# Kernel tuning notes

Hardware: AMD Instinct MI355X
Metric: run time of the kernel (lower is better)

The kernel has to match this reference:

```python
import jax, jax.numpy as jnp
import numpy as np

B, T, C = 2, 2048, 1024
H = 16
D = C // H  # head_dim = 64


def setup_inputs() -> dict:
    key = jax.random.key(0)
    k1, k2, k3, k4, k5 = jax.random.split(key, 5)
    s = 1.0 / np.sqrt(C)
    return {
        "x": jax.random.normal(k1, (B, T, C), dtype=jnp.float32),
        "w_qkv": jax.random.normal(k2, (C, 3 * C), dtype=jnp.float32) * s,
        "b_qkv": jax.random.normal(k3, (3 * C,), dtype=jnp.float32) * 0.01,
        "w_out": jax.random.normal(k4, (C, C), dtype=jnp.float32) * s,
        "b_out": jax.random.normal(k5, (C,), dtype=jnp.float32) * 0.01,
    }


def reference(x, w_qkv, b_qkv, w_out, b_out):
    Bx, Tx, Cx = x.shape
    qkv = x @ w_qkv + b_qkv                      # [B,T,3C]
    qkv = qkv.reshape(Bx, Tx, 3, H, D)
    q, k, v = qkv[:, :, 0], qkv[:, :, 1], qkv[:, :, 2]  # [B,T,H,D]
    # [B,H,T,T] scores with scaling
    scores = jnp.einsum("bqhd,bkhd->bhqk", q, k) / np.sqrt(D).astype(np.float32)
    causal = jnp.tril(jnp.ones((Tx, Tx), dtype=bool))
    scores = jnp.where(causal[None, None], scores, -jnp.inf)
    attn = jax.nn.softmax(scores, axis=-1)
    out = jnp.einsum("bhqk,bkhd->bqhd", attn, v).reshape(Bx, Tx, Cx)
    return out @ w_out + b_out
```

## Files before the change

kernel.cpp:

```cpp
#include <hip/hip_runtime.h>
#include <stdint.h>

typedef unsigned short u16;
typedef __attribute__((ext_vector_type(8))) short bfrag;
typedef __attribute__((ext_vector_type(4))) short bfrag4;
typedef __attribute__((ext_vector_type(4))) float f32x4;

#define MFMA_BF16 __builtin_amdgcn_mfma_f32_16x16x32_bf16

static constexpr int Bc = 2;
static constexpr int Tc = 2048;
static constexpr int Cc = 1024;
static constexpr int Hc = 16;
static constexpr int Dc = 64;
static constexpr int N3 = 3 * Cc;

__device__ __forceinline__ u16 f2bf(float f) {
    union { unsigned int i; float f; } v; v.f = f;
    unsigned int u = v.i;
    u += 0x7fffu + ((u >> 16) & 1u);
    return (u16)(u >> 16);
}
__device__ __forceinline__ unsigned int fbits(float f) {
    union { unsigned int i; float f; } v; v.f = f; return v.i;
}
__device__ __forceinline__ unsigned int pack_bf2(float hi, float lo) {
    return __builtin_amdgcn_perm(fbits(hi), fbits(lo), 0x07060302u);
}

#if __has_builtin(__builtin_amdgcn_mfma_f32_16x16x16bf16_1k)
__device__ __forceinline__ f32x4 MFMA16(bfrag4 a, bfrag4 b, f32x4 c) {
    return __builtin_amdgcn_mfma_f32_16x16x16bf16_1k(a, b, c, 0, 0, 0);
}
#elif __has_builtin(__builtin_amdgcn_mfma_f32_16x16x16_bf16)
__device__ __forceinline__ f32x4 MFMA16(bfrag4 a, bfrag4 b, f32x4 c) {
    return __builtin_amdgcn_mfma_f32_16x16x16_bf16(a, b, c, 0, 0, 0);
}
#else
__device__ __forceinline__ f32x4 MFMA16(bfrag4 a, bfrag4 b, f32x4 c) {
    bfrag a8 = {a[0], a[1], a[2], a[3], 0, 0, 0, 0};
    bfrag b8 = {b[0], b[1], b[2], b[3], 0, 0, 0, 0};
    return MFMA_BF16(a8, b8, c, 0, 0, 0);
}
#endif

__device__ __forceinline__ void async_load16(const u16* g, u16* lds) {
    __builtin_amdgcn_global_load_lds(
        (const __attribute__((address_space(1))) unsigned int*)g,
        (__attribute__((address_space(3))) unsigned int*)lds, 16, 0, 0);
}

__global__ __launch_bounds__(256) void prep(
    const float* __restrict__ x, const float* __restrict__ w_qkv,
    const float* __restrict__ w_out, u16* __restrict__ xb,
    u16* __restrict__ WqkvT, u16* __restrict__ WoutT) {
    __shared__ u16 tile[32][33];
    const int blk = blockIdx.x, tid = threadIdx.x;
    if (blk < 4096) {
        const int i = (blk * 256 + tid) * 4;
        const float4 v = *(const float4*)(x + i);
        ushort4 o;
        o.x = f2bf(v.x); o.y = f2bf(v.y); o.z = f2bf(v.z); o.w = f2bf(v.w);
        *(ushort4*)(xb + i) = o;
        return;
    }
    const float* in; u16* out; int rows, cols, c0, r0;
    if (blk < 4096 + 3072) {
        const int t = blk - 4096;
        in = w_qkv; out = WqkvT; rows = 1024; cols = 3072;
        c0 = (t % 96) * 32; r0 = (t / 96) * 32;
    } else {
        const int t = blk - 7168;
        in = w_out; out = WoutT; rows = 1024; cols = 1024;
        c0 = (t & 31) * 32; r0 = (t >> 5) * 32;
    }
    const int row = tid >> 3;
    const int cg  = (tid & 7) * 4;
    const float4 v = *(const float4*)(in + (size_t)(r0 + row) * cols + c0 + cg);
    tile[cg + 0][row] = f2bf(v.x);
    tile[cg + 1][row] = f2bf(v.y);
    tile[cg + 2][row] = f2bf(v.z);
    tile[cg + 3][row] = f2bf(v.w);
    __syncthreads();
    const int tx = tid & 31, ty = tid >> 5;
    for (int i = 0; i < 4; i++)
        out[(size_t)(c0 + ty + 8 * i) * rows + r0 + tx] = tile[ty + 8 * i][tx];
}

__global__ __launch_bounds__(512, 2) void gemm_qkv(
    const u16* __restrict__ A, const u16* __restrict__ BT,
    const float* __restrict__ bias, u16* __restrict__ outQK,
    u16* __restrict__ Vt) {
    constexpr int Kd = 1024, Nn = 3072, Td = 32;
    extern __shared__ __align__(16) u16 smem[];
    u16* As = smem;
    u16* Bs = smem + 4 * (128 * 32);

    const int tid  = threadIdx.x;
    const int wave = tid >> 6, lane = tid & 63;
    const int quad = lane >> 4, l16 = lane & 15;
    const int wm = wave >> 2, wn = wave & 3;
    const int m0 = blockIdx.y * 128, n0 = blockIdx.x * 384;

    f32x4 acc[4][6];
    #pragma unroll
    for (int i = 0; i < 4; i++)
        #pragma unroll
        for (int j = 0; j < 6; j++)
            acc[i][j] = (f32x4){0.f, 0.f, 0.f, 0.f};

    const int rloc = 2 * (lane >> 3) + ((lane >> 2) & 1);
    const int cg   = ((lane & 3) ^ ((lane >> 3) & 3)) * 8;
    const int rk   = (l16 >> 1) & 3;
    const int rodd = (l16 & 1) * 32;

    const u16* Ag = A  + (size_t)(m0 + wave * 16 + rloc) * Kd + cg;
    const u16* Bg = BT + (size_t)(n0 + wave * 48 + rloc) * Kd + cg;
    u16* ldsA = As + (wave * 16) * 32;
    u16* ldsB = Bs + (wave * 48) * 32;

    int offA[4], offB[6];
    #pragma unroll
    for (int mt = 0; mt < 4; mt++) {
        const int r = wm * 64 + mt * 16 + l16;
        offA[mt] = (r >> 1) * 64 + rodd + (quad ^ rk) * 8;
    }
    #pragma unroll
    for (int nt = 0; nt < 6; nt++) {
        const int r = wn * 96 + nt * 16 + l16;
        offB[nt] = (r >> 1) * 64 + rodd + (quad ^ rk) * 8;
    }

    #define GLD_A(h, bsel)                                                     \
        async_load16(Ag + ((h) << 5), ldsA + (bsel) * (128 * 32));
    #define GLD_B(h, bsel, j)                                                  \
        async_load16(Bg + (size_t)((j) * 16) * Kd + ((h) << 5),                \
                     ldsB + (bsel) * (384 * 32) + (j) * (16 * 32));

    #pragma unroll
    for (int h = 0; h < 3; h++) {
        GLD_A(h, h);
        GLD_B(h, h, 0); GLD_B(h, h, 1); GLD_B(h, h, 2);
    }
    asm volatile("s_waitcnt vmcnt(8)" ::: "memory");
    __builtin_amdgcn_s_barrier();
    asm volatile("" ::: "memory");

    for (int h = 0; h < Td; h++) {
        const int bsel = h & 3;
        const u16* Ab = As + bsel * (128 * 32);
        const u16* Bb = Bs + bsel * (384 * 32);
        const int psel = (h + 3) & 3;

        bfrag af[4], bf0[3];
        #pragma unroll
        for (int mt = 0; mt < 4; mt++) af[mt] = *(const bfrag*)(Ab + offA[mt]);
        #pragma unroll
        for (int nt = 0; nt < 3; nt++) bf0[nt] = *(const bfrag*)(Bb + offB[nt]);
        if (h + 3 < Td) { GLD_A(h + 3, psel); GLD_B(h + 3, psel, 0); }
        __builtin_amdgcn_s_barrier();
        asm volatile("s_waitcnt lgkmcnt(0)" ::: "memory");
        __builtin_amdgcn_sched_barrier(0);
        __builtin_amdgcn_s_setprio(1);
        #pragma unroll
        for (int mt = 0; mt < 4; mt++)
            #pragma unroll
            for (int nt = 0; nt < 3; nt++)
                acc[mt][nt] = MFMA_BF16(af[mt], bf0[nt], acc[mt][nt], 0, 0, 0);
        __builtin_amdgcn_s_setprio(0);
        __builtin_amdgcn_s_barrier();
        asm volatile("" ::: "memory");

        bfrag bf1[3];
        #pragma unroll
        for (int nt = 0; nt < 3; nt++)
            bf1[nt] = *(const bfrag*)(Bb + offB[nt + 3]);
        if (h + 3 < Td) { GLD_B(h + 3, psel, 1); GLD_B(h + 3, psel, 2); }
        if (h <= Td - 4)      asm volatile("s_waitcnt vmcnt(8)" ::: "memory");
        else if (h == Td - 3) asm volatile("s_waitcnt vmcnt(4)" ::: "memory");
        else if (h == Td - 2) asm volatile("s_waitcnt vmcnt(0)" ::: "memory");
        __builtin_amdgcn_s_barrier();
        asm volatile("s_waitcnt lgkmcnt(0)" ::: "memory");
        __builtin_amdgcn_sched_barrier(0);
        __builtin_amdgcn_s_setprio(1);
        #pragma unroll
        for (int mt = 0; mt < 4; mt++)
            #pragma unroll
            for (int nt = 0; nt < 3; nt++)
                acc[mt][nt + 3] = MFMA_BF16(af[mt], bf1[nt], acc[mt][nt + 3], 0, 0, 0);
        __builtin_amdgcn_s_setprio(0);
        __builtin_amdgcn_s_barrier();
        asm volatile("" ::: "memory");
    }
    #undef GLD_A
    #undef GLD_B

    #pragma unroll
    for (int nt = 0; nt < 6; nt++) {
        const int gn = n0 + wn * 96 + nt * 16 + l16;
        const float bv = bias[gn];
        if (gn < 2 * Cc) {
            const float scl = (gn < Cc) ? 0.125f : 1.0f;
            #pragma unroll
            for (int mt = 0; mt < 4; mt++) {
                #pragma unroll
                for (int r = 0; r < 4; r++) {
                    const int gm = m0 + wm * 64 + mt * 16 + quad * 4 + r;
                    outQK[(size_t)gm * Nn + gn] = f2bf((acc[mt][nt][r] + bv) * scl);
                }
            }
        } else {
            const int gnv = gn - 2 * Cc;
            const int h = gnv >> 6, d = gnv & 63;
            #pragma unroll
            for (int mt = 0; mt < 4; mt++) {
                const int gmb = m0 + wm * 64 + mt * 16 + quad * 4;
                const int b = gmb >> 11, trow = gmb & (Tc - 1);
                ushort4 o;
                o.x = f2bf(acc[mt][nt][0] + bv);
                o.y = f2bf(acc[mt][nt][1] + bv);
                o.z = f2bf(acc[mt][nt][2] + bv);
                o.w = f2bf(acc[mt][nt][3] + bv);
                *(ushort4*)(Vt + ((size_t)((b * Hc + h) * Dc + d)) * Tc + trow) = o;
            }
        }
    }
}

__global__ __launch_bounds__(512, 2) void gemm_out(
    const u16* __restrict__ A, const u16* __restrict__ BT,
    const float* __restrict__ bias, float* __restrict__ out,
    int M, int Nn, int K) {
    extern __shared__ __align__(16) u16 smem[];
    u16* As = smem;
    u16* Bs = smem + 3 * (128 * 32);

    const int tid  = threadIdx.x;
    const int wave = tid >> 6, lane = tid & 63;
    const int quad = lane >> 4, l16 = lane & 15;
    const int wm = wave >> 2, wn = wave & 3;
    const int m0 = blockIdx.y * 128, n0 = blockIdx.x * 128;

    f32x4 acc[4][2];
    #pragma unroll
    for (int i = 0; i < 4; i++)
        #pragma unroll
        for (int j = 0; j < 2; j++)
            acc[i][j] = (f32x4){0.f, 0.f, 0.f, 0.f};

    const int rA = lane >> 2;
    const int cA = ((lane & 3) ^ (rA & 3)) * 8;

    const u16* Ag = A  + (size_t)(m0 + wave * 16 + rA) * K + cA;
    const u16* Bg = BT + (size_t)(n0 + wave * 16 + rA) * K + cA;
    u16* ldsA = As + (wave * 16) * 32;
    u16* ldsB = Bs + (wave * 16) * 32;

    const int swz8 = (quad ^ (l16 & 3)) * 8;
    int offA[4], offB[2];
    #pragma unroll
    for (int mt = 0; mt < 4; mt++)
        offA[mt] = (wm * 64 + mt * 16 + l16) * 32 + swz8;
    #pragma unroll
    for (int nt = 0; nt < 2; nt++)
        offB[nt] = (wn * 32 + nt * 16 + l16) * 32 + swz8;

    #define STAGE_O(t, bsel)                                                   \
        {                                                                      \
            const int k0_ = (t) << 5;                                          \
            async_load16(Ag + k0_, ldsA + (bsel) * (128 * 32));                \
            async_load16(Bg + k0_, ldsB + (bsel) * (128 * 32));                \
        }

    STAGE_O(0, 0);
    STAGE_O(1, 1);

    const int T = K >> 5;
    for (int t = 0; t < T; t++) {
        if (t + 1 < T) asm volatile("s_waitcnt vmcnt(2)" ::: "memory");
        else           asm volatile("s_waitcnt vmcnt(0)" ::: "memory");
        __builtin_amdgcn_s_barrier();
        asm volatile("" ::: "memory");
        if (t + 2 < T) { STAGE_O(t + 2, (t + 2) % 3); }

        const u16* Ab = As + (t % 3) * (128 * 32);
        const u16* Bb = Bs + (t % 3) * (128 * 32);
        bfrag af[4], bf[2];
        #pragma unroll
        for (int mt = 0; mt < 4; mt++) af[mt] = *(const bfrag*)(Ab + offA[mt]);
        #pragma unroll
        for (int nt = 0; nt < 2; nt++) bf[nt] = *(const bfrag*)(Bb + offB[nt]);

        __builtin_amdgcn_s_setprio(1);
        #pragma unroll
        for (int mt = 0; mt < 4; mt++)
            #pragma unroll
            for (int nt = 0; nt < 2; nt++)
                acc[mt][nt] = MFMA_BF16(af[mt], bf[nt], acc[mt][nt], 0, 0, 0);
        __builtin_amdgcn_s_setprio(0);
    }
    #undef STAGE_O

    #pragma unroll
    for (int nt = 0; nt < 2; nt++) {
        const int gn = n0 + wn * 32 + nt * 16 + l16;
        const float bv = bias[gn];
        #pragma unroll
        for (int mt = 0; mt < 4; mt++) {
            #pragma unroll
            for (int r = 0; r < 4; r++) {
                const int gm = m0 + wm * 64 + mt * 16 + quad * 4 + r;
                out[(size_t)gm * Nn + gn] = acc[mt][nt][r] + bv;
            }
        }
    }
}

__global__ __launch_bounds__(256, 4) void attn_kernel(
    const u16* __restrict__ QKVp, const u16* __restrict__ Vt,
    u16* __restrict__ Ob) {
    __shared__ __align__(16) u16 KsF[2][64 * 64];
    __shared__ __align__(16) u16 VsF[2][64 * 64];

    const int tid  = threadIdx.x;
    const int wave = tid >> 6, lane = tid & 63;
    const int quad = lane >> 4, l16 = lane & 15;

    const int bh = blockIdx.x & 31;
    const int g5 = blockIdx.x >> 5;
    const int jq = (g5 < 8) ? 31 - g5
                 : (g5 < 16) ? g5 + 8
                 : (g5 < 24) ? 31 - g5
                 : g5 - 24;
    const int b = bh >> 4, h = bh & 15;
    const u16* Qp = QKVp + (size_t)b * Tc * N3 + h * Dc;
    const u16* Kp = Qp + Cc;
    const u16* Vp = Vt + (size_t)bh * Dc * Tc;

    const int qw = jq * 64 + wave * 16;

    const int row8 = lane >> 3;
    const int swz  = ((lane & 7) ^ row8) * 8;
    const int pk0 = ((quad)     ^ (l16 & 7)) * 8;
    const int pk1 = ((quad + 4) ^ (l16 & 7)) * 8;

    bfrag qf0, qf1;
    {
        const u16* qp = Qp + (size_t)(qw + l16) * N3 + quad * 8;
        qf0 = *(const bfrag*)qp;
        qf1 = *(const bfrag*)(qp + 32);
    }

    float l_i = 0.f;
    f32x4 oacc[4];
    #pragma unroll
    for (int g = 0; g < 4; g++) oacc[g] = (f32x4){0.f, 0.f, 0.f, 0.f};

    #define STAGEKV(t, bsel)                                                    \
        {                                                                       \
            const int k0_ = (t) * 64;                                           \
            _Pragma("unroll")                                                   \
            for (int j = 0; j < 2; j++) {                                       \
                const int rr = wave * 16 + j * 8;                               \
                const int gr = rr + row8;                                       \
                async_load16(Kp + (size_t)(k0_ + gr) * N3 + swz,                \
                             &KsF[bsel][rr * 64]);                              \
                async_load16(Vp + (size_t)gr * Tc + k0_ + swz,                  \
                             &VsF[bsel][rr * 64]);                              \
            }                                                                   \
        }

    STAGEKV(0, 0);
    for (int t = 0; t <= jq; t++) {
        __syncthreads();
        if (t < jq) STAGEKV(t + 1, (t + 1) & 1);
        const u16* Kb = KsF[t & 1];
        const u16* Vb = VsF[t & 1];

        f32x4 s[4];
        __builtin_amdgcn_s_setprio(1);
        #pragma unroll
        for (int g = 0; g < 4; g++) {
            const u16* kb = Kb + (g * 16 + l16) * 64;
            bfrag kf0 = *(const bfrag*)(kb + pk0);
            bfrag kf1 = *(const bfrag*)(kb + pk1);
            f32x4 z = (f32x4){0.f, 0.f, 0.f, 0.f};
            z = MFMA_BF16(kf0, qf0, z, 0, 0, 0);
            z = MFMA_BF16(kf1, qf1, z, 0, 0, 0);
            s[g] = z;
        }
        __builtin_amdgcn_s_setprio(0);

        #pragma unroll
        for (int g = 0; g < 4; g++)
            #pragma unroll
            for (int r = 0; r < 4; r++)
                s[g][r] = __expf(s[g][r]);
        if (t == jq) {
            #pragma unroll
            for (int g = 0; g < 4; g++)
                #pragma unroll
                for (int r = 0; r < 4; r++)
                    if (g * 16 + quad * 4 + r > wave * 16 + l16) s[g][r] = 0.f;
        }
        #pragma unroll
        for (int g = 0; g < 4; g++)
            l_i += s[g][0] + s[g][1] + s[g][2] + s[g][3];

        __builtin_amdgcn_s_setprio(1);
        #pragma unroll
        for (int g = 0; g < 4; g++) {
            union { unsigned int u[2]; bfrag4 v; } pf;
            pf.u[0] = pack_bf2(s[g][1], s[g][0]);
            pf.u[1] = pack_bf2(s[g][3], s[g][2]);
            const int vc = ((2 * g + (quad >> 1)) ^ (l16 & 7)) * 8 + (quad & 1) * 4;
            #pragma unroll
            for (int ng = 0; ng < 4; ng++) {
                const bfrag4 vf = *(const bfrag4*)(Vb + (ng * 16 + l16) * 64 + vc);
                oacc[ng] = MFMA16(vf, pf.v, oacc[ng]);
            }
        }
        __builtin_amdgcn_s_setprio(0);
    }
    #undef STAGEKV

    float rs = l_i;
    rs += __shfl_xor(rs, 16);
    rs += __shfl_xor(rs, 32);
    const float inv = 1.f / rs;
    const int q = qw + l16;
    u16* orow = Ob + (size_t)(b * Tc + q) * Cc + h * Dc + quad * 4;
    #pragma unroll
    for (int ng = 0; ng < 4; ng++) {
        ushort4 o;
        o.x = f2bf(oacc[ng][0] * inv);
        o.y = f2bf(oacc[ng][1] * inv);
        o.z = f2bf(oacc[ng][2] * inv);
        o.w = f2bf(oacc[ng][3] * inv);
        *(ushort4*)(orow + ng * 16) = o;
    }
}

extern "C" void kernel_launch(void* const* d_in, const int* in_sizes, int n_in,
                              void* d_out, int out_size, void* d_ws, size_t ws_size,
                              hipStream_t stream) {
    const float* x     = (const float*)d_in[0];
    const float* w_qkv = (const float*)d_in[1];
    const float* b_qkv = (const float*)d_in[2];
    const float* w_out = (const float*)d_in[3];
    const float* b_out = (const float*)d_in[4];
    float* out = (float*)d_out;
    u16* ws  = (u16*)d_ws;

    u16* xb    = ws;
    u16* WqkvT = xb    + (size_t)4096 * 1024;
    u16* WoutT = WqkvT + (size_t)3072 * 1024;
    u16* QKVp  = WoutT + (size_t)1024 * 1024;
    u16* Vt    = QKVp  + (size_t)4096 * 3072;
    u16* Ao    = xb;

    static bool smem_set = false;
    if (!smem_set) {
        hipFuncSetAttribute(reinterpret_cast<const void*>(gemm_qkv),
                            hipFuncAttributeMaxDynamicSharedMemorySize,
                            128 * 1024);
        hipFuncSetAttribute(reinterpret_cast<const void*>(gemm_out),
                            hipFuncAttributeMaxDynamicSharedMemorySize,
                            48 * 1024);
        smem_set = true;
    }

    prep<<<8192, 256, 0, stream>>>(x, w_qkv, w_out, xb, WqkvT, WoutT);
    gemm_qkv<<<dim3(3072 / 384, 4096 / 128), 512, 128 * 1024, stream>>>(
        xb, WqkvT, b_qkv, QKVp, Vt);
    attn_kernel<<<1024, 256, 0, stream>>>(QKVp, Vt, Ao);
    gemm_out<<<dim3(1024 / 128, 4096 / 128), 512, 48 * 1024, stream>>>(
        Ao, WoutT, b_out, out, 4096, 1024, 1024);
}
```

Measured before the change: 173.7 us.

## Software-pipeline QK^T of next tile with softmax and PV of current tile

Restructures the attention main loop so the Q·K^T MFMAs for tile t+1 are issued between the exp/masking and the P·V MFMAs of tile t. Splits K and V staging, triple-buffers K in LDS so K can be prefetched two tiles ahead, and unrolls the loop by two with ping-pong score registers. The aim is to hide exp and VALU work behind matrix-core work and to keep the MFMA pipe busier. In exchange it uses more registers for the second score set and more LDS for the third K buffer, which may reduce occupancy under the 4-blocks-per-CU launch bound.

After: 175.9 us. About the same (+1.2%).

```diff
diff --git a/kernel.cpp b/kernel.cpp
--- a/kernel.cpp
+++ b/kernel.cpp
@@ -319,7 +319,7 @@
 __global__ __launch_bounds__(256, 4) void attn_kernel(
     const u16* __restrict__ QKVp, const u16* __restrict__ Vt,
     u16* __restrict__ Ob) {
-    __shared__ __align__(16) u16 KsF[2][64 * 64];
+    __shared__ __align__(16) u16 KsF[3][64 * 64];
     __shared__ __align__(16) u16 VsF[2][64 * 64];
 
     const int tid  = threadIdx.x;
@@ -356,7 +356,7 @@
     #pragma unroll
     for (int g = 0; g < 4; g++) oacc[g] = (f32x4){0.f, 0.f, 0.f, 0.f};
 
-    #define STAGEKV(t, bsel)                                                    \
+    #define STAGEK_(t, bsel)                                                    \
         {                                                                       \
             const int k0_ = (t) * 64;                                           \
             _Pragma("unroll")                                                   \
@@ -365,64 +365,97 @@
                 const int gr = rr + row8;                                       \
                 async_load16(Kp + (size_t)(k0_ + gr) * N3 + swz,                \
                              &KsF[bsel][rr * 64]);                              \
+            }                                                                   \
+        }
+    #define STAGEV_(t, bsel)                                                    \
+        {                                                                       \
+            const int k0_ = (t) * 64;                                           \
+            _Pragma("unroll")                                                   \
+            for (int j = 0; j < 2; j++) {                                       \
+                const int rr = wave * 16 + j * 8;                               \
+                const int gr = rr + row8;                                       \
                 async_load16(Vp + (size_t)gr * Tc + k0_ + swz,                  \
                              &VsF[bsel][rr * 64]);                              \
             }                                                                   \
         }
-
-    STAGEKV(0, 0);
-    for (int t = 0; t <= jq; t++) {
-        __syncthreads();
-        if (t < jq) STAGEKV(t + 1, (t + 1) & 1);
-        const u16* Kb = KsF[t & 1];
-        const u16* Vb = VsF[t & 1];
-
-        f32x4 s[4];
-        __builtin_amdgcn_s_setprio(1);
-        #pragma unroll
-        for (int g = 0; g < 4; g++) {
-            const u16* kb = Kb + (g * 16 + l16) * 64;
-            bfrag kf0 = *(const bfrag*)(kb + pk0);
-            bfrag kf1 = *(const bfrag*)(kb + pk1);
-            f32x4 z = (f32x4){0.f, 0.f, 0.f, 0.f};
-            z = MFMA_BF16(kf0, qf0, z, 0, 0, 0);
-            z = MFMA_BF16(kf1, qf1, z, 0, 0, 0);
-            s[g] = z;
-        }
-        __builtin_amdgcn_s_setprio(0);
-
-        #pragma unroll
-        for (int g = 0; g < 4; g++)
-            #pragma unroll
-            for (int r = 0; r < 4; r++)
-                s[g][r] = __expf(s[g][r]);
-        if (t == jq) {
-            #pragma unroll
-            for (int g = 0; g < 4; g++)
-                #pragma unroll
-                for (int r = 0; r < 4; r++)
-                    if (g * 16 + quad * 4 + r > wave * 16 + l16) s[g][r] = 0.f;
-        }
-        #pragma unroll
-        for (int g = 0; g < 4; g++)
-            l_i += s[g][0] + s[g][1] + s[g][2] + s[g][3];
-
-        __builtin_amdgcn_s_setprio(1);
-        #pragma unroll
-        for (int g = 0; g < 4; g++) {
-            union { unsigned int u[2]; bfrag4 v; } pf;
-            pf.u[0] = pack_bf2(s[g][1], s[g][0]);
-            pf.u[1] = pack_bf2(s[g][3], s[g][2]);
-            const int vc = ((2 * g + (quad >> 1)) ^ (l16 & 7)) * 8 + (quad & 1) * 4;
-            #pragma unroll
-            for (int ng = 0; ng < 4; ng++) {
-                const bfrag4 vf = *(const bfrag4*)(Vb + (ng * 16 + l16) * 64 + vc);
-                oacc[ng] = MFMA16(vf, pf.v, oacc[ng]);
-            }
-        }
-        __builtin_amdgcn_s_setprio(0);
-    }
-    #undef STAGEKV
+    #define QKSTEP(bsel, SD)                                                    \
+        {                                                                       \
+            const u16* Kb = KsF[bsel];                                          \
+            __builtin_amdgcn_s_setprio(1);                                      \
+            _Pragma("unroll")                                                   \
+            for (int g = 0; g < 4; g++) {                                       \
+                const u16* kb = Kb + (g * 16 + l16) * 64;                       \
+                bfrag kf0 = *(const bfrag*)(kb + pk0);                          \
+                bfrag kf1 = *(const bfrag*)(kb + pk1);                          \
+                f32x4 z = (f32x4){0.f, 0.f, 0.f, 0.f};                          \
+                z = MFMA_BF16(kf0, qf0, z, 0, 0, 0);                            \
+                z = MFMA_BF16(kf1, qf1, z, 0, 0, 0);                            \
+                SD[g] = z;                                                      \
+            }                                                                   \
+            __builtin_amdgcn_s_setprio(0);                                      \
+        }
+    #define ITER(T, SC, SN)                                                     \
+        {                                                                       \
+            const int t_ = (T);                                                 \
+            _Pragma("unroll")                                                   \
+            for (int g = 0; g < 4; g++)                                         \
+                _Pragma("unroll")                                               \
+                for (int r = 0; r < 4; r++)                                     \
+                    SC[g][r] = __expf(SC[g][r]);                                \
+            if (t_ == jq) {                                                     \
+                _Pragma("unroll")                                               \
+                for (int g = 0; g < 4; g++)                                     \
+                    _Pragma("unroll")                                           \
+                    for (int r = 0; r < 4; r++)                                 \
+                        if (g * 16 + quad * 4 + r > wave * 16 + l16)            \
+                            SC[g][r] = 0.f;                                     \
+            }                                                                   \
+            _Pragma("unroll")                                                   \
+            for (int g = 0; g < 4; g++)                                         \
+                l_i += SC[g][0] + SC[g][1] + SC[g][2] + SC[g][3];               \
+            __syncthreads();                                                    \
+            if (t_ + 2 <= jq) STAGEK_(t_ + 2, (t_ + 2) % 3);                    \
+            if (t_ + 1 <= jq) {                                                 \
+                STAGEV_(t_ + 1, (t_ + 1) & 1);                                  \
+                QKSTEP((t_ + 1) % 3, SN);                                       \
+            }                                                                   \
+            const u16* Vb = VsF[t_ & 1];                                        \
+            __builtin_amdgcn_s_setprio(1);                                      \
+            _Pragma("unroll")                                                   \
+            for (int g = 0; g < 4; g++) {                                       \
+                union { unsigned int u[2]; bfrag4 v; } pf;                      \
+                pf.u[0] = pack_bf2(SC[g][1], SC[g][0]);                         \
+                pf.u[1] = pack_bf2(SC[g][3], SC[g][2]);                         \
+                const int vc = ((2 * g + (quad >> 1)) ^ (l16 & 7)) * 8          \
+                               + (quad & 1) * 4;                                \
+                _Pragma("unroll")                                               \
+                for (int ng = 0; ng < 4; ng++) {                                \
+                    const bfrag4 vf =                                           \
+                        *(const bfrag4*)(Vb + (ng * 16 + l16) * 64 + vc);       \
+                    oacc[ng] = MFMA16(vf, pf.v, oacc[ng]);                      \
+                }                                                               \
+            }                                                                   \
+            __builtin_amdgcn_s_setprio(0);                                      \
+        }
+
+    f32x4 sA[4], sB[4];
+    STAGEK_(0, 0);
+    STAGEV_(0, 0);
+    if (jq > 0) STAGEK_(1, 1);
+    __syncthreads();
+    QKSTEP(0, sA);
+
+    int t = 0;
+    for (; t + 1 <= jq; t += 2) {
+        ITER(t, sA, sB);
+        ITER(t + 1, sB, sA);
+    }
+    if (t <= jq) ITER(t, sA, sB);
+
+    #undef ITER
+    #undef QKSTEP
+    #undef STAGEK_
+    #undef STAGEV_
 
     float rs = l_i;
     rs += __shfl_xor(rs, 16);
```

## Load K/V fragments directly from global memory instead of staging through LDS

Applied to the files above, without the earlier changes.

Removes the double-buffered shared-memory staging of K and V tiles and the per-iteration block barrier in the attention kernel. Each wave now reads its MFMA operands straight from global memory (relying on L1/L2 caching), and launch bounds are raised to allow more resident blocks now that no LDS is used. This trades barrier and LDS traffic for redundant global/cache loads across the four waves and exposed load latency without explicit prefetch.

After: 322.6 us. 85.7% more time.

```diff
diff --git a/kernel.cpp b/kernel.cpp
--- a/kernel.cpp
+++ b/kernel.cpp
@@ -316,12 +316,9 @@
     }
 }
 
-__global__ __launch_bounds__(256, 4) void attn_kernel(
+__global__ __launch_bounds__(256, 6) void attn_kernel(
     const u16* __restrict__ QKVp, const u16* __restrict__ Vt,
     u16* __restrict__ Ob) {
-    __shared__ __align__(16) u16 KsF[2][64 * 64];
-    __shared__ __align__(16) u16 VsF[2][64 * 64];
-
     const int tid  = threadIdx.x;
     const int wave = tid >> 6, lane = tid & 63;
     const int quad = lane >> 4, l16 = lane & 15;
@@ -339,11 +336,6 @@
 
     const int qw = jq * 64 + wave * 16;
 
-    const int row8 = lane >> 3;
-    const int swz  = ((lane & 7) ^ row8) * 8;
-    const int pk0 = ((quad)     ^ (l16 & 7)) * 8;
-    const int pk1 = ((quad + 4) ^ (l16 & 7)) * 8;
-
     bfrag qf0, qf1;
     {
         const u16* qp = Qp + (size_t)(qw + l16) * N3 + quad * 8;
@@ -351,43 +343,55 @@
         qf1 = *(const bfrag*)(qp + 32);
     }
 
+    const u16* kb0 = Kp + (size_t)l16 * N3 + quad * 8;
+    const u16* kbase0 = kb0;
+    const u16* kbase1 = kb0 + (size_t)16 * N3;
+    const u16* kbase2 = kb0 + (size_t)32 * N3;
+    const u16* kbase3 = kb0 + (size_t)48 * N3;
+    const u16* vb0 = Vp + (size_t)l16 * Tc + quad * 4;
+    const u16* vbase0 = vb0;
+    const u16* vbase1 = vb0 + (size_t)16 * Tc;
+    const u16* vbase2 = vb0 + (size_t)32 * Tc;
+    const u16* vbase3 = vb0 + (size_t)48 * Tc;
+
     float l_i = 0.f;
     f32x4 oacc[4];
     #pragma unroll
     for (int g = 0; g < 4; g++) oacc[g] = (f32x4){0.f, 0.f, 0.f, 0.f};
 
-    #define STAGEKV(t, bsel)                                                    \
-        {                                                                       \
-            const int k0_ = (t) * 64;                                           \
-            _Pragma("unroll")                                                   \
-            for (int j = 0; j < 2; j++) {                                       \
-                const int rr = wave * 16 + j * 8;                               \
-                const int gr = rr + row8;                                       \
-                async_load16(Kp + (size_t)(k0_ + gr) * N3 + swz,                \
-                             &KsF[bsel][rr * 64]);                              \
-                async_load16(Vp + (size_t)gr * Tc + k0_ + swz,                  \
-                             &VsF[bsel][rr * 64]);                              \
-            }                                                                   \
-        }
-
-    STAGEKV(0, 0);
     for (int t = 0; t <= jq; t++) {
-        __syncthreads();
-        if (t < jq) STAGEKV(t + 1, (t + 1) & 1);
-        const u16* Kb = KsF[t & 1];
-        const u16* Vb = VsF[t & 1];
+        const size_t koff = (size_t)(t * 64) * N3;
+        const int voff = t * 64;
 
         f32x4 s[4];
         __builtin_amdgcn_s_setprio(1);
-        #pragma unroll
-        for (int g = 0; g < 4; g++) {
-            const u16* kb = Kb + (g * 16 + l16) * 64;
-            bfrag kf0 = *(const bfrag*)(kb + pk0);
-            bfrag kf1 = *(const bfrag*)(kb + pk1);
-            f32x4 z = (f32x4){0.f, 0.f, 0.f, 0.f};
-            z = MFMA_BF16(kf0, qf0, z, 0, 0, 0);
-            z = MFMA_BF16(kf1, qf1, z, 0, 0, 0);
-            s[g] = z;
+        {
+            const u16* kb;
+            kb = kbase0 + koff;
+            bfrag k00 = *(const bfrag*)kb, k01 = *(const bfrag*)(kb + 32);
+            kb = kbase1 + koff;
+            bfrag k10 = *(const bfrag*)kb, k11 = *(const bfrag*)(kb + 32);
+            kb = kbase2 + koff;
+            bfrag k20 = *(const bfrag*)kb, k21 = *(const bfrag*)(kb + 32);
+            kb = kbase3 + koff;
+            bfrag k30 = *(const bfrag*)kb, k31 = *(const bfrag*)(kb + 32);
+            f32x4 z;
+            z = (f32x4){0.f, 0.f, 0.f, 0.f};
+            z = MFMA_BF16(k00, qf0, z, 0, 0, 0);
+            z = MFMA_BF16(k01, qf1, z, 0, 0, 0);
+            s[0] = z;
+            z = (f32x4){0.f, 0.f, 0.f, 0.f};
+            z = MFMA_BF16(k10, qf0, z, 0, 0, 0);
+            z = MFMA_BF16(k11, qf1, z, 0, 0, 0);
+            s[1] = z;
+            z = (f32x4){0.f, 0.f, 0.f, 0.f};
+            z = MFMA_BF16(k20, qf0, z, 0, 0, 0);
+            z = MFMA_BF16(k21, qf1, z, 0, 0, 0);
+            s[2] = z;
+            z = (f32x4){0.f, 0.f, 0.f, 0.f};
+            z = MFMA_BF16(k30, qf0, z, 0, 0, 0);
+            z = MFMA_BF16(k31, qf1, z, 0, 0, 0);
+            s[3] = z;
         }
         __builtin_amdgcn_s_setprio(0);
 
@@ -413,16 +417,14 @@
             union { unsigned int u[2]; bfrag4 v; } pf;
             pf.u[0] = pack_bf2(s[g][1], s[g][0]);
             pf.u[1] = pack_bf2(s[g][3], s[g][2]);
-            const int vc = ((2 * g + (quad >> 1)) ^ (l16 & 7)) * 8 + (quad & 1) * 4;
-            #pragma unroll
-            for (int ng = 0; ng < 4; ng++) {
-                const bfrag4 vf = *(const bfrag4*)(Vb + (ng * 16 + l16) * 64 + vc);
-                oacc[ng] = MFMA16(vf, pf.v, oacc[ng]);
-            }
+            const int vg = voff + g * 16;
+            oacc[0] = MFMA16(*(const bfrag4*)(vbase0 + vg), pf.v, oacc[0]);
+            oacc[1] = MFMA16(*(const bfrag4*)(vbase1 + vg), pf.v, oacc[1]);
+            oacc[2] = MFMA16(*(const bfrag4*)(vbase2 + vg), pf.v, oacc[2]);
+            oacc[3] = MFMA16(*(const bfrag4*)(vbase3 + vg), pf.v, oacc[3]);
         }
         __builtin_amdgcn_s_setprio(0);
     }
-    #undef STAGEKV
 
     float rs = l_i;
     rs += __shfl_xor(rs, 16);
```

## Split attention work across waves by key block instead of query rows

Applied to the files above, without the earlier changes.

Each wave now covers all 64 query rows of the block but only its own 16-key slice of every KV tile, so each wave loads one K fragment and one set of V fragments per tile instead of four. Partial row sums and output accumulators are then reduced across the four waves through shared memory at the end. This cuts LDS reads per tile but quadruples the accumulator registers, which is why the occupancy hint drops from 4 to 3 blocks. It also adds several block-wide barriers in the epilogue.

After: 168.5 us. -3.0%, faster.

```diff
diff --git a/kernel.cpp b/kernel.cpp
--- a/kernel.cpp
+++ b/kernel.cpp
@@ -316,7 +316,7 @@
     }
 }
 
-__global__ __launch_bounds__(256, 4) void attn_kernel(
+__global__ __launch_bounds__(256, 3) void attn_kernel(
     const u16* __restrict__ QKVp, const u16* __restrict__ Vt,
     u16* __restrict__ Ob) {
     __shared__ __align__(16) u16 KsF[2][64 * 64];
@@ -337,24 +337,27 @@
     const u16* Kp = Qp + Cc;
     const u16* Vp = Vt + (size_t)bh * Dc * Tc;
 
-    const int qw = jq * 64 + wave * 16;
-
     const int row8 = lane >> 3;
     const int swz  = ((lane & 7) ^ row8) * 8;
     const int pk0 = ((quad)     ^ (l16 & 7)) * 8;
     const int pk1 = ((quad + 4) ^ (l16 & 7)) * 8;
-
-    bfrag qf0, qf1;
-    {
-        const u16* qp = Qp + (size_t)(qw + l16) * N3 + quad * 8;
-        qf0 = *(const bfrag*)qp;
-        qf1 = *(const bfrag*)(qp + 32);
-    }
-
-    float l_i = 0.f;
-    f32x4 oacc[4];
-    #pragma unroll
-    for (int g = 0; g < 4; g++) oacc[g] = (f32x4){0.f, 0.f, 0.f, 0.f};
+    const int vc = ((2 * wave + (quad >> 1)) ^ (l16 & 7)) * 8 + (quad & 1) * 4;
+
+    bfrag qf0[4], qf1[4];
+    #pragma unroll
+    for (int qg = 0; qg < 4; qg++) {
+        const u16* qp = Qp + (size_t)(jq * 64 + qg * 16 + l16) * N3 + quad * 8;
+        qf0[qg] = *(const bfrag*)qp;
+        qf1[qg] = *(const bfrag*)(qp + 32);
+    }
+
+    float l4[4] = {0.f, 0.f, 0.f, 0.f};
+    f32x4 oacc[4][4];
+    #pragma unroll
+    for (int qg = 0; qg < 4; qg++)
+        #pragma unroll
+        for (int ng = 0; ng < 4; ng++)
+            oacc[qg][ng] = (f32x4){0.f, 0.f, 0.f, 0.f};
 
     #define STAGEKV(t, bsel)                                                    \
         {                                                                       \
@@ -377,67 +380,93 @@
         const u16* Kb = KsF[t & 1];
         const u16* Vb = VsF[t & 1];
 
+        const u16* kb = Kb + (wave * 16 + l16) * 64;
+        bfrag kf0 = *(const bfrag*)(kb + pk0);
+        bfrag kf1 = *(const bfrag*)(kb + pk1);
+
         f32x4 s[4];
         __builtin_amdgcn_s_setprio(1);
         #pragma unroll
-        for (int g = 0; g < 4; g++) {
-            const u16* kb = Kb + (g * 16 + l16) * 64;
-            bfrag kf0 = *(const bfrag*)(kb + pk0);
-            bfrag kf1 = *(const bfrag*)(kb + pk1);
+        for (int qg = 0; qg < 4; qg++) {
             f32x4 z = (f32x4){0.f, 0.f, 0.f, 0.f};
-            z = MFMA_BF16(kf0, qf0, z, 0, 0, 0);
-            z = MFMA_BF16(kf1, qf1, z, 0, 0, 0);
-            s[g] = z;
+            z = MFMA_BF16(kf0, qf0[qg], z, 0, 0, 0);
+            z = MFMA_BF16(kf1, qf1[qg], z, 0, 0, 0);
+            s[qg] = z;
         }
         __builtin_amdgcn_s_setprio(0);
 
         #pragma unroll
-        for (int g = 0; g < 4; g++)
+        for (int qg = 0; qg < 4; qg++)
             #pragma unroll
             for (int r = 0; r < 4; r++)
-                s[g][r] = __expf(s[g][r]);
+                s[qg][r] = __expf(s[qg][r]);
         if (t == jq) {
             #pragma unroll
-            for (int g = 0; g < 4; g++)
+            for (int qg = 0; qg < 4; qg++)
                 #pragma unroll
                 for (int r = 0; r < 4; r++)
-                    if (g * 16 + quad * 4 + r > wave * 16 + l16) s[g][r] = 0.f;
-        }
-        #pragma unroll
-        for (int g = 0; g < 4; g++)
-            l_i += s[g][0] + s[g][1] + s[g][2] + s[g][3];
+                    if (wave * 16 + quad * 4 + r > qg * 16 + l16) s[qg][r] = 0.f;
+        }
+        #pragma unroll
+        for (int qg = 0; qg < 4; qg++)
+            l4[qg] += s[qg][0] + s[qg][1] + s[qg][2] + s[qg][3];
+
+        bfrag4 vf[4];
+        #pragma unroll
+        for (int ng = 0; ng < 4; ng++)
+            vf[ng] = *(const bfrag4*)(Vb + (ng * 16 + l16) * 64 + vc);
 
         __builtin_amdgcn_s_setprio(1);
         #pragma unroll
-        for (int g = 0; g < 4; g++) {
+        for (int qg = 0; qg < 4; qg++) {
             union { unsigned int u[2]; bfrag4 v; } pf;
-            pf.u[0] = pack_bf2(s[g][1], s[g][0]);
-            pf.u[1] = pack_bf2(s[g][3], s[g][2]);
-            const int vc = ((2 * g + (quad >> 1)) ^ (l16 & 7)) * 8 + (quad & 1) * 4;
-            #pragma unroll
-            for (int ng = 0; ng < 4; ng++) {
-                const bfrag4 vf = *(const bfrag4*)(Vb + (ng * 16 + l16) * 64 + vc);
-                oacc[ng] = MFMA16(vf, pf.v, oacc[ng]);
-            }
+            pf.u[0] = pack_bf2(s[qg][1], s[qg][0]);
+            pf.u[1] = pack_bf2(s[qg][3], s[qg][2]);
+            #pragma unroll
+            for (int ng = 0; ng < 4; ng++)
+                oacc[qg][ng] = MFMA16(vf[ng], pf.v, oacc[qg][ng]);
         }
         __builtin_amdgcn_s_setprio(0);
     }
     #undef STAGEKV
 
-    float rs = l_i;
-    rs += __shfl_xor(rs, 16);
-    rs += __shfl_xor(rs, 32);
-    const float inv = 1.f / rs;
-    const int q = qw + l16;
-    u16* orow = Ob + (size_t)(b * Tc + q) * Cc + h * Dc + quad * 4;
-    #pragma unroll
-    for (int ng = 0; ng < 4; ng++) {
+    __syncthreads();
+
+    float* lred = (float*)VsF;
+    #pragma unroll
+    for (int qg = 0; qg < 4; qg++)
+        lred[(wave * 4 + qg) * 64 + lane] = l4[qg];
+    __syncthreads();
+    float inv[4];
+    #pragma unroll
+    for (int qg = 0; qg < 4; qg++) {
+        float ls = lred[(0 * 4 + qg) * 64 + lane] + lred[(1 * 4 + qg) * 64 + lane]
+                 + lred[(2 * 4 + qg) * 64 + lane] + lred[(3 * 4 + qg) * 64 + lane];
+        ls += __shfl_xor(ls, 16);
+        ls += __shfl_xor(ls, 32);
+        inv[qg] = 1.f / ls;
+    }
+
+    f32x4* ored = (f32x4*)KsF;
+    #pragma unroll
+    for (int qg = 0; qg < 4; qg++) {
+        __syncthreads();
+        #pragma unroll
+        for (int ng = 0; ng < 4; ng++)
+            ored[(wave * 4 + ng) * 64 + lane] = oacc[qg][ng];
+        __syncthreads();
+        f32x4 a0 = ored[(0 * 4 + wave) * 64 + lane];
+        f32x4 a1 = ored[(1 * 4 + wave) * 64 + lane];
+        f32x4 a2 = ored[(2 * 4 + wave) * 64 + lane];
+        f32x4 a3 = ored[(3 * 4 + wave) * 64 + lane];
+        const int q = jq * 64 + qg * 16 + l16;
+        u16* orow = Ob + (size_t)(b * Tc + q) * Cc + h * Dc + wave * 16 + quad * 4;
         ushort4 o;
-        o.x = f2bf(oacc[ng][0] * inv);
-        o.y = f2bf(oacc[ng][1] * inv);
-        o.z = f2bf(oacc[ng][2] * inv);
-        o.w = f2bf(oacc[ng][3] * inv);
-        *(ushort4*)(orow + ng * 16) = o;
+        o.x = f2bf((a0[0] + a1[0] + a2[0] + a3[0]) * inv[qg]);
+        o.y = f2bf((a0[1] + a1[1] + a2[1] + a3[1]) * inv[qg]);
+        o.z = f2bf((a0[2] + a1[2] + a2[2] + a3[2]) * inv[qg]);
+        o.w = f2bf((a0[3] + a1[3] + a2[3] + a3[3]) * inv[qg]);
+        *(ushort4*)orow = o;
     }
 }
 
```
